# Optimization experiments

Measured on AMD Instinct MI355X. Metric: run time of the kernel, lower is better.

## Reference

```python
import jax, jax.numpy as jnp
import numpy as np

EPS = 1e-5

def _ln(x):
    m = jnp.mean(x, axis=-1, keepdims=True)
    v = jnp.mean((x - m) ** 2, axis=-1, keepdims=True)
    return (x - m) / jnp.sqrt(v + EPS)

def setup_inputs() -> dict:
    key = jax.random.key(0)
    ks = jax.random.split(key, 6)
    B, S, E, H = 2, 2048, 1024, 16
    sd = 1.0 / np.sqrt(E)
    x = jax.random.normal(ks[0], (B, S, E), dtype=jnp.float32)
    w_in = jax.random.normal(ks[1], (3 * E, E), dtype=jnp.float32) * sd
    w_out = jax.random.normal(ks[2], (E, E), dtype=jnp.float32) * sd
    w_fc = jax.random.normal(ks[3], (4 * E, E), dtype=jnp.float32) * sd
    b_fc = jnp.zeros((4 * E,), dtype=jnp.float32)
    w_proj = jax.random.normal(ks[4], (E, 4 * E), dtype=jnp.float32) * (1.0 / np.sqrt(4 * E))
    b_proj = jnp.zeros((E,), dtype=jnp.float32)
    return {"x": x, "w_in": w_in, "w_out": w_out, "w_fc": w_fc,
            "b_fc": b_fc, "w_proj": w_proj, "b_proj": b_proj}

def reference(x, w_in, w_out, w_fc, b_fc, w_proj, b_proj):
    B, S, E = x.shape
    H = 16
    D = E // H
    h = _ln(x)
    qkv = h @ w_in.T                      # [B,S,3E]
    q, k, v = jnp.split(qkv, 3, axis=-1)
    q = q.reshape(B, S, H, D)
    k = k.reshape(B, S, H, D)
    v = v.reshape(B, S, H, D)
    scale = 1.0 / np.sqrt(D)
    scores = jnp.einsum('bqhd,bkhd->bhqk', q, k) * scale  # [B,H,S,S]
    causal = jnp.tril(jnp.ones((S, S), dtype=bool))
    scores = jnp.where(causal, scores, -jnp.inf)
    attn = jax.nn.softmax(scores, axis=-1)
    o = jnp.einsum('bhqk,bkhd->bqhd', attn, v).reshape(B, S, E)
    attn_out = o @ w_out.T
    x2 = x + attn_out                      # residual 1
    h2 = _ln(x2)
    m = jax.nn.relu(h2 @ w_fc.T + b_fc)    # [B,S,4E]
    return (m @ w_proj.T + b_proj) + x2    # residual 2
```

## Files before the change

### kernel.cpp

```cpp
#include <hip/hip_runtime.h>
#include <stdint.h>

#define AS1 __attribute__((address_space(1)))
#define AS3 __attribute__((address_space(3)))

typedef __bf16 bf8_t __attribute__((ext_vector_type(8)));
typedef float f4_t __attribute__((ext_vector_type(4)));
typedef unsigned short ush;

__device__ __forceinline__ ush f2b(float f) {
  unsigned u = __builtin_bit_cast(unsigned, f);
  u += 0x7fffu + ((u >> 16) & 1u);
  return (ush)(u >> 16);
}
__device__ __forceinline__ void unpack8(uint4 u, float* dst) {
  unsigned a0 = u.x, a1 = u.y, a2 = u.z, a3 = u.w;
  dst[0] = __builtin_bit_cast(float, a0 << 16);
  dst[1] = __builtin_bit_cast(float, a0 & 0xffff0000u);
  dst[2] = __builtin_bit_cast(float, a1 << 16);
  dst[3] = __builtin_bit_cast(float, a1 & 0xffff0000u);
  dst[4] = __builtin_bit_cast(float, a2 << 16);
  dst[5] = __builtin_bit_cast(float, a2 & 0xffff0000u);
  dst[6] = __builtin_bit_cast(float, a3 << 16);
  dst[7] = __builtin_bit_cast(float, a3 & 0xffff0000u);
}

__device__ __forceinline__ void ln_row(const float* __restrict__ x,
                                       ush* __restrict__ out, int row, int tid) {
  const float* xr = x + (size_t)row * 1024;
  float4 v = ((const float4*)xr)[tid];
  float s = v.x + v.y + v.z + v.w;
  float q = v.x * v.x + v.y * v.y + v.z * v.z + v.w * v.w;
  for (int o = 32; o; o >>= 1) { s += __shfl_down(s, o); q += __shfl_down(q, o); }
  __shared__ float rs[4], rq[4];
  const int w = tid >> 6;
  if ((tid & 63) == 0) { rs[w] = s; rq[w] = q; }
  __syncthreads();
  s = rs[0] + rs[1] + rs[2] + rs[3];
  q = rq[0] + rq[1] + rq[2] + rq[3];
  const float mean = s * (1.0f / 1024.0f);
  const float var = q * (1.0f / 1024.0f) - mean * mean;
  const float rstd = rsqrtf(var + 1e-5f);
  union { ush u[4]; uint2 d; } p;
  p.u[0] = f2b((v.x - mean) * rstd);
  p.u[1] = f2b((v.y - mean) * rstd);
  p.u[2] = f2b((v.z - mean) * rstd);
  p.u[3] = f2b((v.w - mean) * rstd);
  *(uint2*)(out + (size_t)row * 1024 + tid * 4) = p.d;
}

__global__ __launch_bounds__(256) void f2b_ln(
    const float* __restrict__ w_in, const float* __restrict__ w_out,
    const float* __restrict__ w_fc, const float* __restrict__ w_proj,
    ush* __restrict__ o_in, ush* __restrict__ o_out,
    ush* __restrict__ o_fc, ush* __restrict__ o_proj,
    const float* __restrict__ x, ush* __restrict__ h_b) {
  const int blk = blockIdx.x;
  if (blk >= 12288) {
    ln_row(x, h_b, blk - 12288, threadIdx.x);
    return;
  }
  const float* src;
  ush* dst;
  int base;
  if (blk < 3072) { src = w_in; dst = o_in; base = blk; }
  else if (blk < 4096) { src = w_out; dst = o_out; base = blk - 3072; }
  else if (blk < 8192) { src = w_fc; dst = o_fc; base = blk - 4096; }
  else { src = w_proj; dst = o_proj; base = blk - 8192; }
  const int i = (base * 256 + threadIdx.x) * 4;
  float4 v = *(const float4*)(src + i);
  union { ush u[4]; uint2 d; } p;
  p.u[0] = f2b(v.x); p.u[1] = f2b(v.y); p.u[2] = f2b(v.z); p.u[3] = f2b(v.w);
  *(uint2*)(dst + i) = p.d;
}

__global__ __launch_bounds__(256) void ln_kernel(const float* __restrict__ x,
                                                 ush* __restrict__ out) {
  ln_row(x, out, blockIdx.x, threadIdx.x);
}

template <int EPI>
__global__ __launch_bounds__(512, 2) void gemm8p(
    const ush* __restrict__ A, const ush* __restrict__ Bw,
    int M, int N, int K, int lda, int ldb,
    const float* __restrict__ bias, const float* __restrict__ resid,
    float* __restrict__ outF, ush* __restrict__ outB) {
  __shared__ __align__(16) ush lds[65536];
  ush* const LA0 = lds;
  ush* const LA1 = lds + 16384;
  ush* const LB0 = lds + 32768;
  ush* const LB1 = lds + 49152;

  const int tid = threadIdx.x;
  const int wave = tid >> 6, lane = tid & 63;
  const int wm = wave >> 2, wn = wave & 3;
  const int l16 = lane & 15, quad = lane >> 4;
  const int sw = l16 & 7;
  const int bm = blockIdx.x, bn = blockIdx.y;
  const int bmrow = bm * 256, bnrow = bn * 256;
  const size_t kbase = (size_t)blockIdx.z * (size_t)K;
  const int KT = K >> 6;
  const int nit = KT >> 1;
  const int gcs = (((lane & 7) ^ ((lane >> 3) & 7)) << 3);

  auto stage = [&](const ush* __restrict__ gbase, int blkrow, int ld,
                   ush* dstbase, int t, int h) {
    const int kt = t & (KT - 1);
#pragma unroll
    for (int i2 = 0; i2 < 2; ++i2) {
      const int rr = h * 128 + (wave * 2 + i2) * 8 + (lane >> 3);
      const ush* g = gbase + (size_t)(blkrow + rr) * ld + kbase + kt * 64 + gcs;
      __builtin_amdgcn_global_load_lds(
          (const AS1 void*)g,
          (AS3 void*)(dstbase + h * 8192 + (wave * 2 + i2) * 512), 16, 0, 0);
    }
  };

  f4_t acc[8][4];
#pragma unroll
  for (int i = 0; i < 8; ++i)
#pragma unroll
    for (int j = 0; j < 4; ++j) acc[i][j] = (f4_t){0.f, 0.f, 0.f, 0.f};

  stage(A, bmrow, lda, LA0, 0, 0);
  stage(A, bmrow, lda, LA0, 0, 1);
  stage(Bw, bnrow, ldb, LB0, 0, 0);
  stage(Bw, bnrow, ldb, LB0, 0, 1);
  stage(A, bmrow, lda, LA1, 1, 0);
  asm volatile("s_waitcnt vmcnt(2)" ::: "memory");
  __builtin_amdgcn_s_barrier();

  bf8_t af[4][2], bf[2][2];

  for (int it = 0; it < nit; ++it) {
#pragma unroll
    for (int hf = 0; hf < 2; ++hf) {
      ush* const cA = hf ? LA1 : LA0;
      ush* const cB = hf ? LB1 : LB0;
#pragma unroll
      for (int sub = 0; sub < 4; ++sub) {
        const int p = hf * 4 + sub;
        if (sub == 0) {
#pragma unroll
          for (int m = 0; m < 4; ++m)
#pragma unroll
            for (int kk = 0; kk < 2; ++kk)
              af[m][kk] = *(const bf8_t*)&cA[(wm * 128 + m * 16 + l16) * 64 +
                                            (((kk * 4 + quad) ^ sw) << 3)];
#pragma unroll
          for (int n = 0; n < 2; ++n)
#pragma unroll
            for (int kk = 0; kk < 2; ++kk)
              bf[n][kk] = *(const bf8_t*)&cB[(wn * 64 + n * 16 + l16) * 64 +
                                            (((kk * 4 + quad) ^ sw) << 3)];
        } else if (sub == 1) {
#pragma unroll
          for (int n = 0; n < 2; ++n)
#pragma unroll
            for (int kk = 0; kk < 2; ++kk)
              bf[n][kk] = *(const bf8_t*)&cB[(wn * 64 + (2 + n) * 16 + l16) * 64 +
                                            (((kk * 4 + quad) ^ sw) << 3)];
        } else if (sub == 2) {
#pragma unroll
          for (int m = 0; m < 4; ++m)
#pragma unroll
            for (int kk = 0; kk < 2; ++kk)
              af[m][kk] = *(const bf8_t*)&cA[(wm * 128 + (4 + m) * 16 + l16) * 64 +
                                            (((kk * 4 + quad) ^ sw) << 3)];
#pragma unroll
          for (int n = 0; n < 2; ++n)
#pragma unroll
            for (int kk = 0; kk < 2; ++kk)
              bf[n][kk] = *(const bf8_t*)&cB[(wn * 64 + n * 16 + l16) * 64 +
                                            (((kk * 4 + quad) ^ sw) << 3)];
        } else {
#pragma unroll
          for (int n = 0; n < 2; ++n)
#pragma unroll
            for (int kk = 0; kk < 2; ++kk)
              bf[n][kk] = *(const bf8_t*)&cB[(wn * 64 + (2 + n) * 16 + l16) * 64 +
                                            (((kk * 4 + quad) ^ sw) << 3)];
        }
        if (p == 0) stage(A, bmrow, lda, LA1, 2 * it + 1, 1);
        else if (p == 1) stage(Bw, bnrow, ldb, LB1, 2 * it + 1, 0);
        else if (p == 2) stage(Bw, bnrow, ldb, LB1, 2 * it + 1, 1);
        else if (p == 3) stage(A, bmrow, lda, LA0, 2 * it + 2, 0);
        else if (p == 4) stage(A, bmrow, lda, LA0, 2 * it + 2, 1);
        else if (p == 5) stage(Bw, bnrow, ldb, LB0, 2 * it + 2, 0);
        else if (p == 6) stage(Bw, bnrow, ldb, LB0, 2 * it + 2, 1);
        else stage(A, bmrow, lda, LA1, 2 * it + 3, 0);
        if (sub == 3) asm volatile("s_waitcnt vmcnt(2)" ::: "memory");
        __builtin_amdgcn_s_barrier();
        asm volatile("s_waitcnt lgkmcnt(0)" ::: "memory");
        __builtin_amdgcn_sched_barrier(0);
        __builtin_amdgcn_s_setprio(1);
        const int mo = (sub >= 2) ? 4 : 0;
        const int no = (sub & 1) ? 2 : 0;
#pragma unroll
        for (int m = 0; m < 4; ++m)
#pragma unroll
          for (int n = 0; n < 2; ++n)
#pragma unroll
            for (int kk = 0; kk < 2; ++kk)
              acc[mo + m][no + n] = __builtin_amdgcn_mfma_f32_16x16x32_bf16(
                  af[m][kk], bf[n][kk], acc[mo + m][no + n], 0, 0, 0);
        __builtin_amdgcn_s_setprio(0);
        __builtin_amdgcn_s_barrier();
      }
    }
  }

  asm volatile("s_waitcnt vmcnt(0)" ::: "memory");
  __builtin_amdgcn_s_barrier();

  if (EPI == 0 || EPI == 2) {
    ush* outBz = outB + (size_t)blockIdx.z * ((size_t)M * N);
    ush* eb = lds + wave * 8192;
    float bv[4];
    if (EPI == 2) {
#pragma unroll
      for (int ni = 0; ni < 4; ++ni) bv[ni] = bias[bn * 256 + wn * 64 + ni * 16 + l16];
    }
#pragma unroll
    for (int mi = 0; mi < 8; ++mi)
#pragma unroll
      for (int ni = 0; ni < 4; ++ni)
#pragma unroll
        for (int r = 0; r < 4; ++r) {
          float v = acc[mi][ni][r];
          if (EPI == 2) v = fmaxf(v + bv[ni], 0.0f);
          eb[(mi * 16 + quad * 4 + r) * 64 + ni * 16 + l16] = f2b(v);
        }
    asm volatile("s_waitcnt lgkmcnt(0)" ::: "memory");
#pragma unroll
    for (int j = 0; j < 16; ++j) {
      const int lr = j * 8 + (lane >> 3);
      const int c8 = (lane & 7) * 8;
      uint4 v = *(const uint4*)&eb[lr * 64 + c8];
      *(uint4*)(outBz + (size_t)(bm * 256 + wm * 128 + lr) * N + bn * 256 +
                wn * 64 + c8) = v;
    }
  } else {
#pragma unroll
    for (int mi = 0; mi < 8; ++mi)
#pragma unroll
      for (int ni = 0; ni < 4; ++ni) {
        const int gm0 = bm * 256 + wm * 128 + mi * 16 + quad * 4;
        const int gn = bn * 256 + wn * 64 + ni * 16 + l16;
        const float bv = (EPI == 3) ? bias[gn] : 0.0f;
#pragma unroll
        for (int r = 0; r < 4; ++r) {
          const size_t idx = (size_t)(gm0 + r) * N + gn;
          outF[idx] = acc[mi][ni][r] + bv + resid[idx];
        }
      }
  }
}

__global__ __launch_bounds__(256) void reduce4(const ush* __restrict__ p,
                                               const float* __restrict__ bias,
                                               const float* __restrict__ resid,
                                               float* __restrict__ out) {
  const size_t i = ((size_t)blockIdx.x * 256 + threadIdx.x) * 8;
  const int col = (int)(i & 1023);
  float acc[8];
  float4 r0 = *(const float4*)(resid + i);
  float4 r1 = *(const float4*)(resid + i + 4);
  acc[0] = r0.x + bias[col + 0]; acc[1] = r0.y + bias[col + 1];
  acc[2] = r0.z + bias[col + 2]; acc[3] = r0.w + bias[col + 3];
  acc[4] = r1.x + bias[col + 4]; acc[5] = r1.y + bias[col + 5];
  acc[6] = r1.z + bias[col + 6]; acc[7] = r1.w + bias[col + 7];
#pragma unroll
  for (int z = 0; z < 4; ++z) {
    uint4 u = *(const uint4*)(p + (size_t)z * 4194304 + i);
    float f[8]; unpack8(u, f);
#pragma unroll
    for (int j = 0; j < 8; ++j) acc[j] += f[j];
  }
  *(float4*)(out + i) = *(float4*)acc;
  *(float4*)(out + i + 4) = *(float4*)(acc + 4);
}

template <int EPI, int BM, int MINW>
__global__ __launch_bounds__(256, MINW) void gemm_bt(
    const ush* __restrict__ A, const ush* __restrict__ Bw,
    int M, int N, int K,
    const float* __restrict__ bias, const float* __restrict__ resid,
    float* __restrict__ outF, ush* __restrict__ outB) {
  constexpr int MI = BM / 32;
  constexpr int NCH = (BM + 128) / 16;
  constexpr int PC = NCH / 4;
  constexpr int ASZ = BM * 32;
  __shared__ ush lds[2 * ASZ + 2 * 4096];
  const int tid = threadIdx.x;
  const int wave = tid >> 6, lane = tid & 63;
  const int bm = blockIdx.x, bn = blockIdx.y;
  const int wm = (wave & 1) * (BM / 2), wn = (wave >> 1) * 64;
  const int l16 = lane & 15, quad = lane >> 4;
  const int srow = lane >> 2;
  const int scol = (lane & 3) * 8;

  const ush* Abase = A + (size_t)(bm * BM) * K;
  const ush* Bbase = Bw + (size_t)(bn * 128) * K;

  f4_t acc[MI][4];
#pragma unroll
  for (int i = 0; i < MI; ++i)
#pragma unroll
    for (int j = 0; j < 4; ++j) acc[i][j] = (f4_t){0.f, 0.f, 0.f, 0.f};

  const int kiters = K >> 5;

  auto stage = [&](int k0, int buf) {
    const int kk = k0 * 32;
#pragma unroll
    for (int i = 0; i < PC; ++i) {
      const int c = wave * PC + i;
      if (c < BM / 16) {
        const ush* ga = Abase + (size_t)(c * 16 + srow) * K + kk + scol;
        __builtin_amdgcn_global_load_lds((const AS1 void*)ga,
                                         (AS3 void*)(lds + buf * ASZ + c * 512), 16, 0, 0);
      } else {
        const int c2 = c - BM / 16;
        const ush* gb = Bbase + (size_t)(c2 * 16 + srow) * K + kk + scol;
        __builtin_amdgcn_global_load_lds(
            (const AS1 void*)gb, (AS3 void*)(lds + 2 * ASZ + buf * 4096 + c2 * 512), 16, 0, 0);
      }
    }
  };

  stage(0, 0);
  __syncthreads();
  for (int k0 = 0; k0 < kiters; ++k0) {
    const int cur = k0 & 1;
    if (k0 + 1 < kiters) stage(k0 + 1, cur ^ 1);
    bf8_t af[MI], bfr[4];
#pragma unroll
    for (int mi = 0; mi < MI; ++mi)
      af[mi] = *(const bf8_t*)&lds[cur * ASZ + (wm + mi * 16 + l16) * 32 + quad * 8];
#pragma unroll
    for (int ni = 0; ni < 4; ++ni)
      bfr[ni] = *(const bf8_t*)&lds[2 * ASZ + cur * 4096 + (wn + ni * 16 + l16) * 32 + quad * 8];
#pragma unroll
    for (int mi = 0; mi < MI; ++mi)
#pragma unroll
      for (int ni = 0; ni < 4; ++ni)
        acc[mi][ni] =
            __builtin_amdgcn_mfma_f32_16x16x32_bf16(af[mi], bfr[ni], acc[mi][ni], 0, 0, 0);
    __syncthreads();
  }

  if (EPI == 0 || EPI == 2) {
    ush* eb = lds + wave * ASZ;
#pragma unroll
    for (int mi = 0; mi < MI; ++mi)
#pragma unroll
      for (int ni = 0; ni < 4; ++ni) {
        const int gn = bn * 128 + wn + ni * 16 + l16;
        const float bv = (EPI == 2) ? bias[gn] : 0.0f;
#pragma unroll
        for (int r = 0; r < 4; ++r) {
          float v = acc[mi][ni][r] + bv;
          if (EPI == 2) v = fmaxf(v, 0.0f);
          eb[(mi * 16 + quad * 4 + r) * 64 + ni * 16 + l16] = f2b(v);
        }
      }
#pragma unroll
    for (int j = 0; j < BM / 16; ++j) {
      const int lr = j * 8 + (lane >> 3);
      const int c8 = (lane & 7) * 8;
      uint4 v = *(const uint4*)&eb[lr * 64 + c8];
      *(uint4*)(outB + (size_t)(bm * BM + wm + lr) * N + bn * 128 + wn + c8) = v;
    }
  } else {
#pragma unroll
    for (int mi = 0; mi < MI; ++mi) {
#pragma unroll
      for (int ni = 0; ni < 4; ++ni) {
        const int gm0 = bm * BM + wm + mi * 16 + quad * 4;
        const int gn = bn * 128 + wn + ni * 16 + l16;
        const float bv = (EPI == 3) ? bias[gn] : 0.0f;
#pragma unroll
        for (int r = 0; r < 4; ++r) {
          const size_t idx = (size_t)(gm0 + r) * N + gn;
          outF[idx] = acc[mi][ni][r] + bv + resid[idx];
        }
      }
    }
  }
}

__global__ __launch_bounds__(256) void pack_kv(const ush* __restrict__ qkv,
                                               ush* __restrict__ Kp,
                                               ush* __restrict__ Vp) {
  const int lin = blockIdx.x;
  const int kt = lin & 31, h = (lin >> 5) & 15, b = lin >> 9;
  const int tid = threadIdx.x;
  __shared__ ush Vs[64 * 72];
  const size_t rowbase = (size_t)(b * 2048 + kt * 64) * 3072 + h * 64;
  ush* Kt = Kp + (size_t)lin * 4096;
  ush* Vt = Vp + (size_t)lin * 4096;

  const int r0 = tid >> 3, cin = tid & 7;
#pragma unroll
  for (int it = 0; it < 2; ++it) {
    const int r = r0 + it * 32;
    uint4 ku = *(const uint4*)(qkv + rowbase + (size_t)r * 3072 + 1024 + cin * 8);
    float f[8]; unpack8(ku, f);
    union { ush us[8]; uint4 v; } pk;
#pragma unroll
    for (int j = 0; j < 8; ++j) pk.us[j] = f2b(f[j] * 0.18033688f);
    *(uint4*)(Kt + (size_t)(r * 8 + (cin ^ (r & 7))) * 8) = pk.v;
    uint4 vu = *(const uint4*)(qkv + rowbase + (size_t)r * 3072 + 2048 + cin * 8);
    *(uint4*)&Vs[r * 72 + cin * 8] = vu;
  }
  __syncthreads();
#pragma unroll
  for (int oc2 = 0; oc2 < 2; ++oc2) {
    const int oc = tid * 2 + oc2;
    const int d = oc >> 3, c = oc & 7;
    const int k0 = 8 * (c ^ (d & 7));
    union { ush us[8]; uint4 v; } pk;
#pragma unroll
    for (int j = 0; j < 8; ++j) pk.us[j] = Vs[(k0 + j) * 72 + d];
    *(uint4*)(Vt + (size_t)oc * 8) = pk.v;
  }
}

__global__ __launch_bounds__(256, 4) void attn_kernel(const ush* __restrict__ qkv,
                                                      const ush* __restrict__ Kp,
                                                      const ush* __restrict__ Vp,
                                                      ush* __restrict__ o) {
  const int lin = blockIdx.x;
  const int b = lin & 1, h = (lin >> 1) & 15;
  const int sg = lin >> 5, jg = sg >> 3, kg = sg & 7;
  const int tq = (jg == 0) ? (31 - 2 * kg)
               : (jg == 1) ? (2 * kg)
               : (jg == 2) ? (30 - 2 * kg)
                           : (2 * kg + 1);
  const int tid = threadIdx.x;
  const int wave = tid >> 6, lane = tid & 63;
  const int l15 = lane & 15, quad = lane >> 4;

  __shared__ __align__(16) ush Ks[2 * 4096];
  __shared__ __align__(16) ush Vt[2 * 4096];
  __shared__ __align__(16) ush Ps[64 * 64];

  bf8_t qf[2];
  {
    const int qrow = b * 2048 + tq * 64 + wave * 16 + l15;
#pragma unroll
    for (int s = 0; s < 2; ++s) {
      union { uint4 u; bf8_t v; } pk;
      pk.u = *(const uint4*)(qkv + (size_t)qrow * 3072 + h * 64 + s * 32 + quad * 8);
      qf[s] = pk.v;
    }
  }

  float m_s = -1e30f, l_part = 0.f;
  f4_t O[4];
#pragma unroll
  for (int j = 0; j < 4; ++j) O[j] = (f4_t){0.f, 0.f, 0.f, 0.f};

  const int qw0 = tq * 64 + wave * 16;
  const int swz = (l15 & 7) * 8;
  const int prow = wave * 16 + l15;
  const int pswz = (prow & 7) << 3;
  const size_t tile0 = (size_t)((b * 16 + h) * 32) * 4096;
  const ush* const KT0 = Kp + tile0;
  const ush* const VT0 = Vp + tile0;
  const int sA = (wave * 2 + 0) * 512 + lane * 8;
  const int sB = (wave * 2 + 1) * 512 + lane * 8;

  uint4 ka, kb, va, vb;
  ka = *(const uint4*)(KT0 + sA); kb = *(const uint4*)(KT0 + sB);
  va = *(const uint4*)(VT0 + sA); vb = *(const uint4*)(VT0 + sB);
  *(uint4*)(Ks + sA) = ka; *(uint4*)(Ks + sB) = kb;
  *(uint4*)(Vt + sA) = va; *(uint4*)(Vt + sB) = vb;
  if (tq >= 1) {
    ka = *(const uint4*)(KT0 + 4096 + sA); kb = *(const uint4*)(KT0 + 4096 + sB);
    va = *(const uint4*)(VT0 + 4096 + sA); vb = *(const uint4*)(VT0 + 4096 + sB);
  }
  asm volatile("s_waitcnt lgkmcnt(0)" ::: "memory");
  __builtin_amdgcn_s_barrier();

  for (int kt = 0; kt <= tq; ++kt) {
    const int cur = (kt & 1) * 4096;
    const int nxt = 4096 - cur;
    if (kt + 1 <= tq) {
      *(uint4*)(Ks + nxt + sA) = ka; *(uint4*)(Ks + nxt + sB) = kb;
      *(uint4*)(Vt + nxt + sA) = va; *(uint4*)(Vt + nxt + sB) = vb;
      if (kt + 2 <= tq) {
        const ush* K2 = KT0 + (size_t)(kt + 2) * 4096;
        const ush* V2 = VT0 + (size_t)(kt + 2) * 4096;
        ka = *(const uint4*)(K2 + sA); kb = *(const uint4*)(K2 + sB);
        va = *(const uint4*)(V2 + sA); vb = *(const uint4*)(V2 + sB);
      }
    }

    bf8_t vf[4][2];
#pragma unroll
    for (int n4 = 0; n4 < 4; ++n4)
#pragma unroll
      for (int s = 0; s < 2; ++s)
        vf[n4][s] = *(const bf8_t*)&Vt[cur + (n4 * 16 + l15) * 64 + (((4 * s + quad) * 8) ^ swz)];

    f4_t S[4];
#pragma unroll
    for (int mi = 0; mi < 4; ++mi) S[mi] = (f4_t){0.f, 0.f, 0.f, 0.f};
    __builtin_amdgcn_s_setprio(1);
#pragma unroll
    for (int s = 0; s < 2; ++s)
#pragma unroll
      for (int mi = 0; mi < 4; ++mi) {
        bf8_t kf = *(const bf8_t*)&Ks[cur + (mi * 16 + l15) * 64 + (((4 * s + quad) * 8) ^ swz)];
        S[mi] = __builtin_amdgcn_mfma_f32_16x16x32_bf16(kf, qf[s], S[mi], 0, 0, 0);
      }
    __builtin_amdgcn_s_setprio(0);

    if (kt == tq) {
#pragma unroll
      for (int mi = 0; mi < 4; ++mi)
#pragma unroll
        for (int r = 0; r < 4; ++r) {
          const int kg2 = kt * 64 + mi * 16 + quad * 4 + r;
          const int qg = qw0 + l15;
          if (kg2 > qg) S[mi][r] = -1e30f;
        }
    }

    float t0 = fmaxf(fmaxf(S[0][0], S[0][1]), fmaxf(S[0][2], S[0][3]));
    float t1 = fmaxf(fmaxf(S[1][0], S[1][1]), fmaxf(S[1][2], S[1][3]));
    float t2 = fmaxf(fmaxf(S[2][0], S[2][1]), fmaxf(S[2][2], S[2][3]));
    float t3 = fmaxf(fmaxf(S[3][0], S[3][1]), fmaxf(S[3][2], S[3][3]));
    float mx = fmaxf(fmaxf(t0, t1), fmaxf(t2, t3));
    mx = fmaxf(mx, __shfl_xor(mx, 16));
    mx = fmaxf(mx, __shfl_xor(mx, 32));

    if (!__all(mx - m_s <= 8.0f)) {
      const float mn = fmaxf(m_s, mx);
      const float dm = m_s - mn;
      float alpha;
      asm("v_exp_f32 %0, %1" : "=v"(alpha) : "v"(dm));
      float ar[4];
#pragma unroll
      for (int r = 0; r < 4; ++r) ar[r] = __shfl(alpha, quad * 4 + r);
#pragma unroll
      for (int n4 = 0; n4 < 4; ++n4)
#pragma unroll
        for (int r = 0; r < 4; ++r) O[n4][r] *= ar[r];
      l_part *= alpha;
      m_s = mn;
    }

    float sum = 0.f;
#pragma unroll
    for (int mi = 0; mi < 4; ++mi)
#pragma unroll
      for (int r = 0; r < 4; ++r) {
        const float z = S[mi][r] - m_s;
        float pv;
        asm("v_exp_f32 %0, %1" : "=v"(pv) : "v"(z));
        S[mi][r] = pv;
        sum += pv;
      }
    l_part += sum;

#pragma unroll
    for (int mi = 0; mi < 4; ++mi) {
      uint2 w2;
      asm("v_cvt_pk_bf16_f32 %0, %1, %2" : "=v"(w2.x) : "v"(S[mi][0]), "v"(S[mi][1]));
      asm("v_cvt_pk_bf16_f32 %0, %1, %2" : "=v"(w2.y) : "v"(S[mi][2]), "v"(S[mi][3]));
      *(uint2*)&Ps[prow * 64 + ((mi * 16 + quad * 4) ^ pswz)] = w2;
    }

    bf8_t pf[2];
#pragma unroll
    for (int s = 0; s < 2; ++s)
      pf[s] = *(const bf8_t*)&Ps[prow * 64 + ((s * 32 + quad * 8) ^ pswz)];
    __builtin_amdgcn_s_setprio(1);
#pragma unroll
    for (int n4 = 0; n4 < 4; ++n4)
#pragma unroll
      for (int s = 0; s < 2; ++s)
        O[n4] = __builtin_amdgcn_mfma_f32_16x16x32_bf16(pf[s], vf[n4][s], O[n4], 0, 0, 0);
    __builtin_amdgcn_s_setprio(0);

    asm volatile("s_waitcnt lgkmcnt(0)" ::: "memory");
    __builtin_amdgcn_s_barrier();
  }

  float l_s = l_part;
  l_s += __shfl_xor(l_s, 16);
  l_s += __shfl_xor(l_s, 32);
  const float rc = 1.0f / l_s;
  float rr[4];
#pragma unroll
  for (int r = 0; r < 4; ++r) rr[r] = __shfl(rc, quad * 4 + r);
#pragma unroll
  for (int n4 = 0; n4 < 4; ++n4)
#pragma unroll
    for (int r = 0; r < 4; ++r) {
      const int qg = tq * 64 + wave * 16 + quad * 4 + r;
      o[(size_t)(b * 2048 + qg) * 1024 + h * 64 + n4 * 16 + l15] = f2b(O[n4][r] * rr[r]);
    }
}

extern "C" void kernel_launch(void* const* d_in, const int* in_sizes, int n_in,
                              void* d_out, int out_size, void* d_ws, size_t ws_size,
                              hipStream_t stream) {
  const float* x = (const float*)d_in[0];
  const float* w_in = (const float*)d_in[1];
  const float* w_out = (const float*)d_in[2];
  const float* w_fc = (const float*)d_in[3];
  const float* b_fc = (const float*)d_in[4];
  const float* w_proj = (const float*)d_in[5];
  const float* b_proj = (const float*)d_in[6];
  float* out = (float*)d_out;

  char* ws = (char*)d_ws;
  ush* w_in_b = (ush*)(ws);
  ush* w_out_b = (ush*)(ws + 6291456);
  ush* h_b = (ush*)(ws + 8388608);
  ush* Kp = (ush*)(ws + 16777216);
  ush* Vp = (ush*)(ws + 25165824);
  ush* Pp = (ush*)(ws);
  ush* w_fc_b = (ush*)(ws + 33554432);
  ush* w_proj_b = (ush*)(ws + 41943040);
  float* x2 = (float*)(ws + 50331648);
  ush* qkv_b = (ush*)(ws + 67108864);
  ush* m_b = (ush*)(ws + 67108864);
  ush* o_b = (ush*)(ws + 92274688);

  f2b_ln<<<16384, 256, 0, stream>>>(w_in, w_out, w_fc, w_proj,
                                    w_in_b, w_out_b, w_fc_b, w_proj_b, x, h_b);

  gemm8p<0><<<dim3(16, 12), 512, 0, stream>>>(
      h_b, w_in_b, 4096, 3072, 1024, 1024, 1024, nullptr, nullptr, nullptr, qkv_b);

  pack_kv<<<1024, 256, 0, stream>>>(qkv_b, Kp, Vp);

  attn_kernel<<<1024, 256, 0, stream>>>(qkv_b, Kp, Vp, o_b);

  gemm_bt<1, 64, 4><<<dim3(64, 8), 256, 0, stream>>>(
      o_b, w_out_b, 4096, 1024, 1024, nullptr, x, x2, nullptr);

  ln_kernel<<<4096, 256, 0, stream>>>(x2, h_b);

  gemm8p<2><<<dim3(16, 16), 512, 0, stream>>>(
      h_b, w_fc_b, 4096, 4096, 1024, 1024, 1024, b_fc, nullptr, nullptr, m_b);

  gemm8p<0><<<dim3(16, 4, 4), 512, 0, stream>>>(
      m_b, w_proj_b, 4096, 1024, 1024, 4096, 4096, nullptr, nullptr, nullptr, Pp);

  reduce4<<<2048, 256, 0, stream>>>(Pp, b_proj, x2, out);
}
```

Baseline: 294.9 us.

## Split attention KV loop across two wave groups with LDS merge

Doubles the attention block to 512 threads and splits the key tiles between two groups of four waves, even tiles to one group and odd tiles to the other. Each group keeps its own online-softmax state, and the two partial results are merged through LDS at the end. K/V tile loads switch from register staging to direct global-to-LDS loads. This shortens the serial KV loop per block, at the cost of extra LDS, a final merge step, and idle waves on odd tile counts.

```diff
diff --git a/kernel.cpp b/kernel.cpp
--- a/kernel.cpp
+++ b/kernel.cpp
@@ -427,7 +427,7 @@
   }
 }
 
-__global__ __launch_bounds__(256, 4) void attn_kernel(const ush* __restrict__ qkv,
+__global__ __launch_bounds__(512, 2) void attn_kernel(const ush* __restrict__ qkv,
                                                       const ush* __restrict__ Kp,
                                                       const ush* __restrict__ Vp,
                                                       ush* __restrict__ o) {
@@ -440,15 +440,18 @@
                            : (2 * kg + 1);
   const int tid = threadIdx.x;
   const int wave = tid >> 6, lane = tid & 63;
+  const int g = wave >> 2;
+  const int wq = wave & 3;
   const int l15 = lane & 15, quad = lane >> 4;
 
-  __shared__ __align__(16) ush Ks[2 * 4096];
-  __shared__ __align__(16) ush Vt[2 * 4096];
-  __shared__ __align__(16) ush Ps[64 * 64];
+  __shared__ __align__(16) ush lds[40960];
+  ush* const Ksg = lds + g * 8192;
+  ush* const Vtg = lds + 16384 + g * 8192;
+  ush* const Psg = lds + 32768 + g * 4096;
 
   bf8_t qf[2];
   {
-    const int qrow = b * 2048 + tq * 64 + wave * 16 + l15;
+    const int qrow = b * 2048 + tq * 64 + wq * 16 + l15;
 #pragma unroll
     for (int s = 0; s < 2; ++s) {
       union { uint4 u; bf8_t v; } pk;
@@ -462,148 +465,183 @@
 #pragma unroll
   for (int j = 0; j < 4; ++j) O[j] = (f4_t){0.f, 0.f, 0.f, 0.f};
 
-  const int qw0 = tq * 64 + wave * 16;
+  const int qw0 = tq * 64 + wq * 16;
   const int swz = (l15 & 7) * 8;
-  const int prow = wave * 16 + l15;
+  const int prow = wq * 16 + l15;
   const int pswz = (prow & 7) << 3;
   const size_t tile0 = (size_t)((b * 16 + h) * 32) * 4096;
-  const ush* const KT0 = Kp + tile0;
-  const ush* const VT0 = Vp + tile0;
-  const int sA = (wave * 2 + 0) * 512 + lane * 8;
-  const int sB = (wave * 2 + 1) * 512 + lane * 8;
-
-  uint4 ka, kb, va, vb;
-  ka = *(const uint4*)(KT0 + sA); kb = *(const uint4*)(KT0 + sB);
-  va = *(const uint4*)(VT0 + sA); vb = *(const uint4*)(VT0 + sB);
-  *(uint4*)(Ks + sA) = ka; *(uint4*)(Ks + sB) = kb;
-  *(uint4*)(Vt + sA) = va; *(uint4*)(Vt + sB) = vb;
-  if (tq >= 1) {
-    ka = *(const uint4*)(KT0 + 4096 + sA); kb = *(const uint4*)(KT0 + 4096 + sB);
-    va = *(const uint4*)(VT0 + 4096 + sA); vb = *(const uint4*)(VT0 + 4096 + sB);
-  }
-  asm volatile("s_waitcnt lgkmcnt(0)" ::: "memory");
+
+  if (g <= tq) {
+    const ush* Ktile = Kp + tile0 + (size_t)g * 4096;
+    const ush* Vtile = Vp + tile0 + (size_t)g * 4096;
+#pragma unroll
+    for (int i = 0; i < 2; ++i) {
+      const int seg = wq * 2 + i;
+      __builtin_amdgcn_global_load_lds((const AS1 void*)(Ktile + seg * 512 + lane * 8),
+                                       (AS3 void*)(Ksg + seg * 512), 16, 0, 0);
+      __builtin_amdgcn_global_load_lds((const AS1 void*)(Vtile + seg * 512 + lane * 8),
+                                       (AS3 void*)(Vtg + seg * 512), 16, 0, 0);
+    }
+  }
+  asm volatile("s_waitcnt vmcnt(0)" ::: "memory");
   __builtin_amdgcn_s_barrier();
 
-  for (int kt = 0; kt <= tq; ++kt) {
-    const int cur = (kt & 1) * 4096;
+  const int nit = (tq >> 1) + 1;
+  for (int j = 0; j < nit; ++j) {
+    const int kt = 2 * j + g;
+    const int cur = (j & 1) * 4096;
     const int nxt = 4096 - cur;
-    if (kt + 1 <= tq) {
-      *(uint4*)(Ks + nxt + sA) = ka; *(uint4*)(Ks + nxt + sB) = kb;
-      *(uint4*)(Vt + nxt + sA) = va; *(uint4*)(Vt + nxt + sB) = vb;
-      if (kt + 2 <= tq) {
-        const ush* K2 = KT0 + (size_t)(kt + 2) * 4096;
-        const ush* V2 = VT0 + (size_t)(kt + 2) * 4096;
-        ka = *(const uint4*)(K2 + sA); kb = *(const uint4*)(K2 + sB);
-        va = *(const uint4*)(V2 + sA); vb = *(const uint4*)(V2 + sB);
-      }
-    }
-
-    bf8_t vf[4][2];
-#pragma unroll
-    for (int n4 = 0; n4 < 4; ++n4)
+    const bool act = (kt <= tq);
+    if (kt + 2 <= tq) {
+      const ush* Ktile = Kp + tile0 + (size_t)(kt + 2) * 4096;
+      const ush* Vtile = Vp + tile0 + (size_t)(kt + 2) * 4096;
+#pragma unroll
+      for (int i = 0; i < 2; ++i) {
+        const int seg = wq * 2 + i;
+        __builtin_amdgcn_global_load_lds((const AS1 void*)(Ktile + seg * 512 + lane * 8),
+                                         (AS3 void*)(Ksg + nxt + seg * 512), 16, 0, 0);
+        __builtin_amdgcn_global_load_lds((const AS1 void*)(Vtile + seg * 512 + lane * 8),
+                                         (AS3 void*)(Vtg + nxt + seg * 512), 16, 0, 0);
+      }
+    }
+
+    if (act) {
+      bf8_t vf[4][2];
+#pragma unroll
+      for (int n4 = 0; n4 < 4; ++n4)
+#pragma unroll
+        for (int s = 0; s < 2; ++s)
+          vf[n4][s] = *(const bf8_t*)&Vtg[cur + (n4 * 16 + l15) * 64 + (((4 * s + quad) * 8) ^ swz)];
+
+      f4_t S[4];
+#pragma unroll
+      for (int mi = 0; mi < 4; ++mi) S[mi] = (f4_t){0.f, 0.f, 0.f, 0.f};
+      __builtin_amdgcn_s_setprio(1);
 #pragma unroll
       for (int s = 0; s < 2; ++s)
-        vf[n4][s] = *(const bf8_t*)&Vt[cur + (n4 * 16 + l15) * 64 + (((4 * s + quad) * 8) ^ swz)];
-
-    f4_t S[4];
-#pragma unroll
-    for (int mi = 0; mi < 4; ++mi) S[mi] = (f4_t){0.f, 0.f, 0.f, 0.f};
-    __builtin_amdgcn_s_setprio(1);
-#pragma unroll
-    for (int s = 0; s < 2; ++s)
+#pragma unroll
+        for (int mi = 0; mi < 4; ++mi) {
+          bf8_t kf = *(const bf8_t*)&Ksg[cur + (mi * 16 + l15) * 64 + (((4 * s + quad) * 8) ^ swz)];
+          S[mi] = __builtin_amdgcn_mfma_f32_16x16x32_bf16(kf, qf[s], S[mi], 0, 0, 0);
+        }
+      __builtin_amdgcn_s_setprio(0);
+
+      if (kt == tq) {
+#pragma unroll
+        for (int mi = 0; mi < 4; ++mi)
+#pragma unroll
+          for (int r = 0; r < 4; ++r) {
+            const int kg2 = kt * 64 + mi * 16 + quad * 4 + r;
+            const int qg = qw0 + l15;
+            if (kg2 > qg) S[mi][r] = -1e30f;
+          }
+      }
+
+      float t0 = fmaxf(fmaxf(S[0][0], S[0][1]), fmaxf(S[0][2], S[0][3]));
+      float t1 = fmaxf(fmaxf(S[1][0], S[1][1]), fmaxf(S[1][2], S[1][3]));
+      float t2 = fmaxf(fmaxf(S[2][0], S[2][1]), fmaxf(S[2][2], S[2][3]));
+      float t3 = fmaxf(fmaxf(S[3][0], S[3][1]), fmaxf(S[3][2], S[3][3]));
+      float mx = fmaxf(fmaxf(t0, t1), fmaxf(t2, t3));
+      mx = fmaxf(mx, __shfl_xor(mx, 16));
+      mx = fmaxf(mx, __shfl_xor(mx, 32));
+
+      if (!__all(mx - m_s <= 8.0f)) {
+        const float mn = fmaxf(m_s, mx);
+        const float dm = m_s - mn;
+        float alpha;
+        asm("v_exp_f32 %0, %1" : "=v"(alpha) : "v"(dm));
+        float ar[4];
+#pragma unroll
+        for (int r = 0; r < 4; ++r) ar[r] = __shfl(alpha, quad * 4 + r);
+#pragma unroll
+        for (int n4 = 0; n4 < 4; ++n4)
+#pragma unroll
+          for (int r = 0; r < 4; ++r) O[n4][r] *= ar[r];
+        l_part *= alpha;
+        m_s = mn;
+      }
+
+      float sum = 0.f;
+#pragma unroll
+      for (int mi = 0; mi < 4; ++mi)
+#pragma unroll
+        for (int r = 0; r < 4; ++r) {
+          const float z = S[mi][r] - m_s;
+          float pv;
+          asm("v_exp_f32 %0, %1" : "=v"(pv) : "v"(z));
+          S[mi][r] = pv;
+          sum += pv;
+        }
+      l_part += sum;
+
 #pragma unroll
       for (int mi = 0; mi < 4; ++mi) {
-        bf8_t kf = *(const bf8_t*)&Ks[cur + (mi * 16 + l15) * 64 + (((4 * s + quad) * 8) ^ swz)];
-        S[mi] = __builtin_amdgcn_mfma_f32_16x16x32_bf16(kf, qf[s], S[mi], 0, 0, 0);
-      }
-    __builtin_amdgcn_s_setprio(0);
-
-    if (kt == tq) {
-#pragma unroll
-      for (int mi = 0; mi < 4; ++mi)
-#pragma unroll
-        for (int r = 0; r < 4; ++r) {
-          const int kg2 = kt * 64 + mi * 16 + quad * 4 + r;
-          const int qg = qw0 + l15;
-          if (kg2 > qg) S[mi][r] = -1e30f;
-        }
-    }
-
-    float t0 = fmaxf(fmaxf(S[0][0], S[0][1]), fmaxf(S[0][2], S[0][3]));
-    float t1 = fmaxf(fmaxf(S[1][0], S[1][1]), fmaxf(S[1][2], S[1][3]));
-    float t2 = fmaxf(fmaxf(S[2][0], S[2][1]), fmaxf(S[2][2], S[2][3]));
-    float t3 = fmaxf(fmaxf(S[3][0], S[3][1]), fmaxf(S[3][2], S[3][3]));
-    float mx = fmaxf(fmaxf(t0, t1), fmaxf(t2, t3));
-    mx = fmaxf(mx, __shfl_xor(mx, 16));
-    mx = fmaxf(mx, __shfl_xor(mx, 32));
-
-    if (!__all(mx - m_s <= 8.0f)) {
-      const float mn = fmaxf(m_s, mx);
-      const float dm = m_s - mn;
-      float alpha;
-      asm("v_exp_f32 %0, %1" : "=v"(alpha) : "v"(dm));
-      float ar[4];
-#pragma unroll
-      for (int r = 0; r < 4; ++r) ar[r] = __shfl(alpha, quad * 4 + r);
+        uint2 w2;
+        asm("v_cvt_pk_bf16_f32 %0, %1, %2" : "=v"(w2.x) : "v"(S[mi][0]), "v"(S[mi][1]));
+        asm("v_cvt_pk_bf16_f32 %0, %1, %2" : "=v"(w2.y) : "v"(S[mi][2]), "v"(S[mi][3]));
+        *(uint2*)&Psg[prow * 64 + ((mi * 16 + quad * 4) ^ pswz)] = w2;
+      }
+
+      bf8_t pf[2];
+#pragma unroll
+      for (int s = 0; s < 2; ++s)
+        pf[s] = *(const bf8_t*)&Psg[prow * 64 + ((s * 32 + quad * 8) ^ pswz)];
+      __builtin_amdgcn_s_setprio(1);
 #pragma unroll
       for (int n4 = 0; n4 < 4; ++n4)
 #pragma unroll
-        for (int r = 0; r < 4; ++r) O[n4][r] *= ar[r];
-      l_part *= alpha;
-      m_s = mn;
-    }
-
-    float sum = 0.f;
-#pragma unroll
-    for (int mi = 0; mi < 4; ++mi)
-#pragma unroll
-      for (int r = 0; r < 4; ++r) {
-        const float z = S[mi][r] - m_s;
-        float pv;
-        asm("v_exp_f32 %0, %1" : "=v"(pv) : "v"(z));
-        S[mi][r] = pv;
-        sum += pv;
-      }
-    l_part += sum;
-
-#pragma unroll
-    for (int mi = 0; mi < 4; ++mi) {
-      uint2 w2;
-      asm("v_cvt_pk_bf16_f32 %0, %1, %2" : "=v"(w2.x) : "v"(S[mi][0]), "v"(S[mi][1]));
-      asm("v_cvt_pk_bf16_f32 %0, %1, %2" : "=v"(w2.y) : "v"(S[mi][2]), "v"(S[mi][3]));
-      *(uint2*)&Ps[prow * 64 + ((mi * 16 + quad * 4) ^ pswz)] = w2;
-    }
-
-    bf8_t pf[2];
-#pragma unroll
-    for (int s = 0; s < 2; ++s)
-      pf[s] = *(const bf8_t*)&Ps[prow * 64 + ((s * 32 + quad * 8) ^ pswz)];
-    __builtin_amdgcn_s_setprio(1);
-#pragma unroll
-    for (int n4 = 0; n4 < 4; ++n4)
-#pragma unroll
-      for (int s = 0; s < 2; ++s)
-        O[n4] = __builtin_amdgcn_mfma_f32_16x16x32_bf16(pf[s], vf[n4][s], O[n4], 0, 0, 0);
-    __builtin_amdgcn_s_setprio(0);
-
-    asm volatile("s_waitcnt lgkmcnt(0)" ::: "memory");
+        for (int s = 0; s < 2; ++s)
+          O[n4] = __builtin_amdgcn_mfma_f32_16x16x32_bf16(pf[s], vf[n4][s], O[n4], 0, 0, 0);
+      __builtin_amdgcn_s_setprio(0);
+    }
+
+    asm volatile("s_waitcnt vmcnt(0)" ::: "memory");
     __builtin_amdgcn_s_barrier();
   }
 
   float l_s = l_part;
   l_s += __shfl_xor(l_s, 16);
   l_s += __shfl_xor(l_s, 32);
-  const float rc = 1.0f / l_s;
-  float rr[4];
-#pragma unroll
-  for (int r = 0; r < 4; ++r) rr[r] = __shfl(rc, quad * 4 + r);
-#pragma unroll
-  for (int n4 = 0; n4 < 4; ++n4)
+
+  float* MO = (float*)lds;
+  float* Mm = (float*)(lds + 8192);
+  float* Ml = (float*)(lds + 8320);
+  if (g == 1) {
+#pragma unroll
+    for (int n4 = 0; n4 < 4; ++n4)
+#pragma unroll
+      for (int r = 0; r < 4; ++r)
+        MO[(wq * 16 + quad * 4 + r) * 64 + n4 * 16 + l15] = O[n4][r];
+    if (quad == 0) { Mm[wq * 16 + l15] = m_s; Ml[wq * 16 + l15] = l_s; }
+  }
+  __syncthreads();
+  if (g == 0) {
+    float m1r[4], l1r[4];
 #pragma unroll
     for (int r = 0; r < 4; ++r) {
-      const int qg = tq * 64 + wave * 16 + quad * 4 + r;
-      o[(size_t)(b * 2048 + qg) * 1024 + h * 64 + n4 * 16 + l15] = f2b(O[n4][r] * rr[r]);
-    }
+      m1r[r] = __shfl(m_s, quad * 4 + r);
+      l1r[r] = __shfl(l_s, quad * 4 + r);
+    }
+#pragma unroll
+    for (int r = 0; r < 4; ++r) {
+      const int row = wq * 16 + quad * 4 + r;
+      const float m2 = Mm[row], l2 = Ml[row];
+      const float mm = fmaxf(m1r[r], m2);
+      const float d1 = m1r[r] - mm, d2 = m2 - mm;
+      float a1, a2;
+      asm("v_exp_f32 %0, %1" : "=v"(a1) : "v"(d1));
+      asm("v_exp_f32 %0, %1" : "=v"(a2) : "v"(d2));
+      const float rc = 1.0f / (l1r[r] * a1 + l2 * a2);
+      const float c1 = a1 * rc, c2 = a2 * rc;
+      const int qg = tq * 64 + row;
+#pragma unroll
+      for (int n4 = 0; n4 < 4; ++n4) {
+        const float o2 = MO[row * 64 + n4 * 16 + l15];
+        o[(size_t)(b * 2048 + qg) * 1024 + h * 64 + n4 * 16 + l15] =
+            f2b(O[n4][r] * c1 + o2 * c2);
+      }
+    }
+  }
 }
 
 extern "C" void kernel_launch(void* const* d_in, const int* in_sizes, int n_in,
@@ -640,7 +678,7 @@
 
   pack_kv<<<1024, 256, 0, stream>>>(qkv_b, Kp, Vp);
 
-  attn_kernel<<<1024, 256, 0, stream>>>(qkv_b, Kp, Vp, o_b);
+  attn_kernel<<<1024, 512, 0, stream>>>(qkv_b, Kp, Vp, o_b);
 
   gemm_bt<1, 64, 4><<<dim3(64, 8), 256, 0, stream>>>(
       o_b, w_out_b, 4096, 1024, 1024, nullptr, x, x2, nullptr);
```

Measured after the change: 308.2 us. 4.5% more time.
